# Performance work log

Measured on AMD Instinct MI355X. Metric: run time of the kernel, lower is better.

The kernel has to match this reference:

```python
import jax, jax.numpy as jnp
import numpy as np
from jax import lax

B, H, W = 512, 128, 128
ARCH = [1, 4096, 4096, 4096, 4096]
CONV_THRESH = 0.0
GRAPH_THRESH = 0.8
EMBED_DIM = 1


def setup_inputs() -> dict:
    key = jax.random.key(0)
    ks = jax.random.split(key, 16)
    inp = {
        "x": jax.random.normal(ks[0], (B, 1, H, W), dtype=jnp.float32),
        "conv_w": jax.random.normal(ks[1], (1, 1, 2, 2), dtype=jnp.float32) * 0.5,
        "conv_b": jax.random.normal(ks[2], (1,), dtype=jnp.float32) * 0.1,
        "rotation": jax.random.normal(ks[3], (EMBED_DIM, EMBED_DIM), dtype=jnp.float32),
        "entangle": jax.random.normal(ks[4], (EMBED_DIM, EMBED_DIM), dtype=jnp.float32),
    }
    # Linear params, torch convention W: [out_f, in_f]
    for i, (fi, fo) in enumerate(zip(ARCH[:-1], ARCH[1:])):
        inp[f"W{i+1}"] = jax.random.normal(ks[5 + 2 * i], (fo, fi), dtype=jnp.float32) / np.sqrt(fi)
        inp[f"b{i+1}"] = jax.random.normal(ks[6 + 2 * i], (fo,), dtype=jnp.float32) * 0.01
    return inp


def _forward(x, conv_w, conv_b, rotation, entangle, W1, b1, W2, b2, W3, b3, W4, b4):
    # ConvFilter: 2x2 valid conv, sigmoid(logits - thresh), mean over C,H,W -> [B]
    logits = lax.conv_general_dilated(
        x, conv_w, window_strides=(1, 1), padding="VALID",
        dimension_numbers=("NCHW", "OIHW", "NCHW"))
    logits = logits + conv_b.reshape(1, -1, 1, 1)
    conv_out = jax.nn.sigmoid(logits - CONV_THRESH).mean(axis=(1, 2, 3))  # [B]
    conv_vec = conv_out[:, None]  # [B, 1] -> embed_dim forced to 1

    # ClassicalSelfAttention (embed_dim = 1)
    q = conv_vec @ rotation                      # [B, 1]
    k = conv_vec @ entangle                      # [B, 1]
    scores = jax.nn.softmax((q @ k.T) / np.sqrt(EMBED_DIM).astype(np.float32), axis=-1)  # [B, B]
    attn_out = scores @ conv_vec                 # [B, 1]

    # tanh MLP stack
    out = attn_out
    acts = []
    for Wl, bl in ((W1, b1), (W2, b2), (W3, b3), (W4, b4)):
        out = jnp.tanh(out @ Wl.T + bl)          # [B, out_f]
        acts.append(out)

    # Vectorized fidelity adjacency over equal-shaped layer activations:
    # normalized Gram matrix squared, thresholded (replaces the O(L^2)
    # Python loop with .item() syncs in the source).
    S = jnp.stack([a.reshape(-1) for a in acts])                  # [L, B*4096]
    S_hat = S / (jnp.linalg.norm(S, axis=1, keepdims=True) + 1e-12)
    fid = (S_hat @ S_hat.T) ** 2                                   # [L, L]
    L = len(acts)
    weights = jnp.where(fid >= GRAPH_THRESH, 1.0, 0.0) * (1.0 - jnp.eye(L, dtype=fid.dtype))
    return out, weights


def reference(x, conv_w, conv_b, rotation, entangle, W1, b1, W2, b2, W3, b3, W4, b4):
    return _forward(x, conv_w, conv_b, rotation, entangle, W1, b1, W2, b2, W3, b3, W4, b4)
```

## Files before the change

### kernel.cpp

```cpp
#include <hip/hip_runtime.h>
#include <cmath>


#define NEL (512 * 4096)

typedef float  floatx4 __attribute__((ext_vector_type(4)));
typedef _Float16 halfx8 __attribute__((ext_vector_type(8)));
typedef _Float16 halfx4 __attribute__((ext_vector_type(4)));

__global__ __launch_bounds__(256) void conv_mean_kernel(
    const float* __restrict__ x, const float* __restrict__ cw,
    const float* __restrict__ cb, float* __restrict__ c_out)
{
  __shared__ float sbuf[4];
  const int b = blockIdx.x;
  const float w00 = cw[0], w01 = cw[1], w10 = cw[2], w11 = cw[3];
  const float bias = cb[0];
  const float* xb = x + (size_t)b * 128 * 128;
  float acc = 0.f;
  for (int idx = threadIdx.x; idx < 127 * 127; idx += 256) {
    int i = idx / 127;
    int j = idx - i * 127;
    const float* p = xb + i * 128 + j;
    float v = w00 * p[0] + w01 * p[1] + w10 * p[128] + w11 * p[129] + bias;
    acc += 1.0f / (1.0f + __expf(-v));
  }
  #pragma unroll
  for (int off = 32; off > 0; off >>= 1) acc += __shfl_down(acc, off, 64);
  const int lane = threadIdx.x & 63, wv = threadIdx.x >> 6;
  if (lane == 0) sbuf[wv] = acc;
  __syncthreads();
  if (threadIdx.x == 0)
    c_out[b] = (sbuf[0] + sbuf[1] + sbuf[2] + sbuf[3]) * (1.0f / 16129.0f);
}

__global__ __launch_bounds__(64) void attn_kernel(
    const float* __restrict__ c, const float* __restrict__ rot,
    const float* __restrict__ ent, float* __restrict__ attn)
{
  const int i = blockIdx.x;
  const int lane = threadIdx.x;
  const float t = rot[0] * ent[0] * c[i];
  float vals[8], cj[8];
  float mx = -1e30f;
  #pragma unroll
  for (int u = 0; u < 8; ++u) {
    float cv = c[lane + u * 64];
    cj[u] = cv;
    vals[u] = t * cv;
    mx = fmaxf(mx, vals[u]);
  }
  #pragma unroll
  for (int off = 32; off > 0; off >>= 1) mx = fmaxf(mx, __shfl_down(mx, off, 64));
  mx = __shfl(mx, 0, 64);
  float se = 0.f, sw = 0.f;
  #pragma unroll
  for (int u = 0; u < 8; ++u) {
    float e = __expf(vals[u] - mx);
    se += e;
    sw += e * cj[u];
  }
  #pragma unroll
  for (int off = 32; off > 0; off >>= 1) {
    se += __shfl_down(se, off, 64);
    sw += __shfl_down(sw, off, 64);
  }
  if (lane == 0) attn[i] = sw / se;
}

__global__ __launch_bounds__(256) void layer1_kernel(
    const float* __restrict__ attn, const float* __restrict__ W1,
    const float* __restrict__ b1, float* __restrict__ act1)
{
  const int o = blockIdx.x * 256 + threadIdx.x;
  const int i = blockIdx.y;
  act1[(size_t)i * 4096 + o] = tanhf(attn[i] * W1[o] + b1[o]);
}

#define BM 128
#define BN 128
#define BK 32
#define LDK 40

template<bool FUSE>
__global__ __launch_bounds__(256) void gemm_tanh_kernel(
    const float* __restrict__ A, const float* __restrict__ W,
    const float* __restrict__ bias, float* __restrict__ C)
{
  __shared__ _Float16 As[BM][LDK];
  __shared__ _Float16 Ws[BN][LDK];
  const int K = 4096, N = 4096;
  const int tid  = threadIdx.x;
  const int lane = tid & 63;
  const int wave = tid >> 6;
  const int wm = (wave >> 1) * 64;
  const int wn = (wave & 1) * 64;
  const int q  = lane >> 4;
  const int ml = lane & 15;
  const int tileM = blockIdx.y * BM;
  const int tileN = blockIdx.x * BN;
  const int Kslice = K / gridDim.z;
  const int kbeg = blockIdx.z * Kslice;
  float* Cb = FUSE ? C : C + (size_t)blockIdx.z * NEL;

  floatx4 acc[4][4] = {};

  for (int k0 = kbeg; k0 < kbeg + Kslice; k0 += BK) {
    __syncthreads();
    #pragma unroll
    for (int u = 0; u < 4; ++u) {
      const int id = tid + u * 256;
      const int r  = id >> 3;
      const int cc = (id & 7) << 2;
      const float4 av = *reinterpret_cast<const float4*>(
          A + (size_t)(tileM + r) * K + k0 + cc);
      halfx4 ha = { (_Float16)av.x, (_Float16)av.y, (_Float16)av.z, (_Float16)av.w };
      *reinterpret_cast<halfx4*>(&As[r][cc]) = ha;
      const float4 wvv = *reinterpret_cast<const float4*>(
          W + (size_t)(tileN + r) * K + k0 + cc);
      halfx4 hw = { (_Float16)wvv.x, (_Float16)wvv.y, (_Float16)wvv.z, (_Float16)wvv.w };
      *reinterpret_cast<halfx4*>(&Ws[r][cc]) = hw;
    }
    __syncthreads();

    halfx8 af[4], bf[4];
    #pragma unroll
    for (int i = 0; i < 4; ++i)
      af[i] = *reinterpret_cast<const halfx8*>(&As[wm + i * 16 + ml][q * 8]);
    #pragma unroll
    for (int j = 0; j < 4; ++j)
      bf[j] = *reinterpret_cast<const halfx8*>(&Ws[wn + j * 16 + ml][q * 8]);

    #pragma unroll
    for (int i = 0; i < 4; ++i)
      #pragma unroll
      for (int j = 0; j < 4; ++j)
        acc[i][j] = __builtin_amdgcn_mfma_f32_16x16x32_f16(af[i], bf[j], acc[i][j], 0, 0, 0);
  }

  #pragma unroll
  for (int i = 0; i < 4; ++i) {
    const int row0 = tileM + wm + i * 16 + q * 4;
    #pragma unroll
    for (int j = 0; j < 4; ++j) {
      const int col = tileN + wn + j * 16 + ml;
      if (FUSE) {
        const float bv = bias[col];
        #pragma unroll
        for (int r = 0; r < 4; ++r)
          Cb[(size_t)(row0 + r) * N + col] = tanhf(acc[i][j][r] + bv);
      } else {
        #pragma unroll
        for (int r = 0; r < 4; ++r)
          Cb[(size_t)(row0 + r) * N + col] = acc[i][j][r];
      }
    }
  }
}

__global__ __launch_bounds__(256) void combine_tanh_kernel(
    const float* __restrict__ part, const float* __restrict__ bias,
    float* __restrict__ outp)
{
  const int i4 = blockIdx.x * 256 + threadIdx.x;
  const floatx4* p4 = (const floatx4*)part;
  floatx4 s = p4[i4] + p4[NEL / 4 + i4] + p4[2 * (NEL / 4) + i4] + p4[3 * (NEL / 4) + i4];
  const floatx4 bv = ((const floatx4*)bias)[i4 & 1023];
  floatx4 o;
  #pragma unroll
  for (int r = 0; r < 4; ++r) o[r] = tanhf(s[r] + bv[r]);
  ((floatx4*)outp)[i4] = o;
}

__global__ __launch_bounds__(256) void fid_dots_kernel(
    const float* __restrict__ a1, const float* __restrict__ a2,
    const float* __restrict__ a3, const float* __restrict__ a4,
    float* __restrict__ D)
{
  __shared__ float sred[4][10];
  float s[10] = {0, 0, 0, 0, 0, 0, 0, 0, 0, 0};
  const int n4 = NEL / 4;
  const int stride = gridDim.x * blockDim.x;
  const floatx4* p1 = (const floatx4*)a1;
  const floatx4* p2 = (const floatx4*)a2;
  const floatx4* p3 = (const floatx4*)a3;
  const floatx4* p4 = (const floatx4*)a4;
  for (int i = blockIdx.x * 256 + threadIdx.x; i < n4; i += stride) {
    floatx4 v1 = p1[i], v2 = p2[i], v3 = p3[i], v4 = p4[i];
    #pragma unroll
    for (int r = 0; r < 4; ++r) {
      s[0] += v1[r] * v1[r]; s[1] += v1[r] * v2[r]; s[2] += v1[r] * v3[r];
      s[3] += v1[r] * v4[r]; s[4] += v2[r] * v2[r]; s[5] += v2[r] * v3[r];
      s[6] += v2[r] * v4[r]; s[7] += v3[r] * v3[r]; s[8] += v3[r] * v4[r];
      s[9] += v4[r] * v4[r];
    }
  }
  const int lane = threadIdx.x & 63, wv = threadIdx.x >> 6;
  #pragma unroll
  for (int p = 0; p < 10; ++p) {
    float v = s[p];
    #pragma unroll
    for (int off = 32; off > 0; off >>= 1) v += __shfl_down(v, off, 64);
    if (lane == 0) sred[wv][p] = v;
  }
  __syncthreads();
  if (threadIdx.x < 10) {
    float v = sred[0][threadIdx.x] + sred[1][threadIdx.x] +
              sred[2][threadIdx.x] + sred[3][threadIdx.x];
    atomicAdd(&D[threadIdx.x * 16], v);
  }
}

__global__ void finalize_kernel(const float* __restrict__ D, float* __restrict__ wout)
{
  const int i = threadIdx.x;
  if (i >= 16) return;
  const int p = i >> 2, qq = i & 3;
  const int a = p < qq ? p : qq;
  const int b = p < qq ? qq : p;
  const int base[4] = {0, 4, 7, 9};
  const float dpq = D[(base[a] + (b - a)) * 16];
  const float npv = sqrtf(D[base[p] * 16]) + 1e-12f;
  const float nqv = sqrtf(D[base[qq] * 16]) + 1e-12f;
  const float ch = dpq / (npv * nqv);
  const float fid = ch * ch;
  wout[i] = (fid >= 0.8f && p != qq) ? 1.0f : 0.0f;
}

extern "C" void kernel_launch(void* const* d_in, const int* in_sizes, int n_in,
                              void* d_out, int out_size, void* d_ws, size_t ws_size,
                              hipStream_t stream)
{
  const float* x   = (const float*)d_in[0];
  const float* cw  = (const float*)d_in[1];
  const float* cb  = (const float*)d_in[2];
  const float* rot = (const float*)d_in[3];
  const float* ent = (const float*)d_in[4];
  const float* W1  = (const float*)d_in[5];
  const float* b1  = (const float*)d_in[6];
  const float* W2  = (const float*)d_in[7];
  const float* b2  = (const float*)d_in[8];
  const float* W3  = (const float*)d_in[9];
  const float* b3  = (const float*)d_in[10];
  const float* W4  = (const float*)d_in[11];
  const float* b4  = (const float*)d_in[12];
  float* out = (float*)d_out;

  char*  ws    = (char*)d_ws;
  float* c_buf = (float*)(ws + 0);
  float* attn  = (float*)(ws + 2048);
  float* D     = (float*)(ws + 4096);
  float* act1  = (float*)(ws + 8192);
  float* act2  = act1 + NEL;
  float* act3  = act2 + NEL;
  float* part  = act3 + NEL;
  float* wout  = out + NEL;

  const size_t need = 8192 + (size_t)3 * NEL * 4 + (size_t)4 * NEL * 4;
  const bool splitk = ws_size >= need;

  hipMemsetAsync(D, 0, 10 * 16 * sizeof(float), stream);
  conv_mean_kernel<<<512, 256, 0, stream>>>(x, cw, cb, c_buf);
  attn_kernel<<<512, 64, 0, stream>>>(c_buf, rot, ent, attn);
  layer1_kernel<<<dim3(16, 512), 256, 0, stream>>>(attn, W1, b1, act1);

  if (splitk) {
    dim3 g(4096 / BN, 512 / BM, 4);
    const int cgrid = NEL / 4 / 256;
    gemm_tanh_kernel<false><<<g, 256, 0, stream>>>(act1, W2, nullptr, part);
    combine_tanh_kernel<<<cgrid, 256, 0, stream>>>(part, b2, act2);
    gemm_tanh_kernel<false><<<g, 256, 0, stream>>>(act2, W3, nullptr, part);
    combine_tanh_kernel<<<cgrid, 256, 0, stream>>>(part, b3, act3);
    gemm_tanh_kernel<false><<<g, 256, 0, stream>>>(act3, W4, nullptr, part);
    combine_tanh_kernel<<<cgrid, 256, 0, stream>>>(part, b4, out);
  } else {
    dim3 g(4096 / BN, 512 / BM, 1);
    gemm_tanh_kernel<true><<<g, 256, 0, stream>>>(act1, W2, b2, act2);
    gemm_tanh_kernel<true><<<g, 256, 0, stream>>>(act2, W3, b3, act3);
    gemm_tanh_kernel<true><<<g, 256, 0, stream>>>(act3, W4, b4, out);
  }

  fid_dots_kernel<<<256, 256, 0, stream>>>(act1, act2, act3, out, D);
  finalize_kernel<<<1, 64, 0, stream>>>(D, wout);
}
```

Baseline: 429.1 us.

## Register-prefetch GEMM tiles and add 8-way split-K path

```diff
diff --git a/kernel.cpp b/kernel.cpp
--- a/kernel.cpp
+++ b/kernel.cpp
@@ -6,7 +6,6 @@
 
 typedef float  floatx4 __attribute__((ext_vector_type(4)));
 typedef _Float16 halfx8 __attribute__((ext_vector_type(8)));
-typedef _Float16 halfx4 __attribute__((ext_vector_type(4)));
 
 __global__ __launch_bounds__(256) void conv_mean_kernel(
     const float* __restrict__ x, const float* __restrict__ cw,
@@ -101,27 +100,48 @@
   const int tileN = blockIdx.x * BN;
   const int Kslice = K / gridDim.z;
   const int kbeg = blockIdx.z * Kslice;
+  const int kend = kbeg + Kslice;
   float* Cb = FUSE ? C : C + (size_t)blockIdx.z * NEL;
 
   floatx4 acc[4][4] = {};
 
-  for (int k0 = kbeg; k0 < kbeg + Kslice; k0 += BK) {
+  const int r0  = tid >> 2;
+  const int cc0 = (tid & 3) << 3;
+
+  float4 pa[4], pw[4];
+  auto load_tile = [&](int k0) {
+    #pragma unroll
+    for (int u = 0; u < 2; ++u) {
+      const float* ap = A + (size_t)(tileM + r0 + u * 64) * K + k0 + cc0;
+      pa[2 * u]     = *reinterpret_cast<const float4*>(ap);
+      pa[2 * u + 1] = *reinterpret_cast<const float4*>(ap + 4);
+      const float* wp = W + (size_t)(tileN + r0 + u * 64) * K + k0 + cc0;
+      pw[2 * u]     = *reinterpret_cast<const float4*>(wp);
+      pw[2 * u + 1] = *reinterpret_cast<const float4*>(wp + 4);
+    }
+  };
+  auto store_tile = [&]() {
+    #pragma unroll
+    for (int u = 0; u < 2; ++u) {
+      halfx8 ha = { (_Float16)pa[2*u].x, (_Float16)pa[2*u].y,
+                    (_Float16)pa[2*u].z, (_Float16)pa[2*u].w,
+                    (_Float16)pa[2*u+1].x, (_Float16)pa[2*u+1].y,
+                    (_Float16)pa[2*u+1].z, (_Float16)pa[2*u+1].w };
+      *reinterpret_cast<halfx8*>(&As[r0 + u * 64][cc0]) = ha;
+      halfx8 hw = { (_Float16)pw[2*u].x, (_Float16)pw[2*u].y,
+                    (_Float16)pw[2*u].z, (_Float16)pw[2*u].w,
+                    (_Float16)pw[2*u+1].x, (_Float16)pw[2*u+1].y,
+                    (_Float16)pw[2*u+1].z, (_Float16)pw[2*u+1].w };
+      *reinterpret_cast<halfx8*>(&Ws[r0 + u * 64][cc0]) = hw;
+    }
+  };
+
+  load_tile(kbeg);
+  for (int k0 = kbeg; k0 < kend; k0 += BK) {
     __syncthreads();
-    #pragma unroll
-    for (int u = 0; u < 4; ++u) {
-      const int id = tid + u * 256;
-      const int r  = id >> 3;
-      const int cc = (id & 7) << 2;
-      const float4 av = *reinterpret_cast<const float4*>(
-          A + (size_t)(tileM + r) * K + k0 + cc);
-      halfx4 ha = { (_Float16)av.x, (_Float16)av.y, (_Float16)av.z, (_Float16)av.w };
-      *reinterpret_cast<halfx4*>(&As[r][cc]) = ha;
-      const float4 wvv = *reinterpret_cast<const float4*>(
-          W + (size_t)(tileN + r) * K + k0 + cc);
-      halfx4 hw = { (_Float16)wvv.x, (_Float16)wvv.y, (_Float16)wvv.z, (_Float16)wvv.w };
-      *reinterpret_cast<halfx4*>(&Ws[r][cc]) = hw;
-    }
+    store_tile();
     __syncthreads();
+    if (k0 + BK < kend) load_tile(k0 + BK);
 
     halfx8 af[4], bf[4];
     #pragma unroll
@@ -158,13 +178,16 @@
   }
 }
 
+template<int S>
 __global__ __launch_bounds__(256) void combine_tanh_kernel(
     const float* __restrict__ part, const float* __restrict__ bias,
     float* __restrict__ outp)
 {
   const int i4 = blockIdx.x * 256 + threadIdx.x;
   const floatx4* p4 = (const floatx4*)part;
-  floatx4 s = p4[i4] + p4[NEL / 4 + i4] + p4[2 * (NEL / 4) + i4] + p4[3 * (NEL / 4) + i4];
+  floatx4 s = p4[i4];
+  #pragma unroll
+  for (int z = 1; z < S; ++z) s += p4[(size_t)z * (NEL / 4) + i4];
   const floatx4 bv = ((const floatx4*)bias)[i4 & 1023];
   floatx4 o;
   #pragma unroll
@@ -256,23 +279,32 @@
   float* part  = act3 + NEL;
   float* wout  = out + NEL;
 
-  const size_t need = 8192 + (size_t)3 * NEL * 4 + (size_t)4 * NEL * 4;
-  const bool splitk = ws_size >= need;
+  const size_t base_need = 8192 + (size_t)3 * NEL * 4;
+  const bool sk8 = ws_size >= base_need + (size_t)8 * NEL * 4;
+  const bool sk4 = ws_size >= base_need + (size_t)4 * NEL * 4;
 
   hipMemsetAsync(D, 0, 10 * 16 * sizeof(float), stream);
   conv_mean_kernel<<<512, 256, 0, stream>>>(x, cw, cb, c_buf);
   attn_kernel<<<512, 64, 0, stream>>>(c_buf, rot, ent, attn);
   layer1_kernel<<<dim3(16, 512), 256, 0, stream>>>(attn, W1, b1, act1);
 
-  if (splitk) {
+  const int cgrid = NEL / 4 / 256;
+  if (sk8) {
+    dim3 g(4096 / BN, 512 / BM, 8);
+    gemm_tanh_kernel<false><<<g, 256, 0, stream>>>(act1, W2, nullptr, part);
+    combine_tanh_kernel<8><<<cgrid, 256, 0, stream>>>(part, b2, act2);
+    gemm_tanh_kernel<false><<<g, 256, 0, stream>>>(act2, W3, nullptr, part);
+    combine_tanh_kernel<8><<<cgrid, 256, 0, stream>>>(part, b3, act3);
+    gemm_tanh_kernel<false><<<g, 256, 0, stream>>>(act3, W4, nullptr, part);
+    combine_tanh_kernel<8><<<cgrid, 256, 0, stream>>>(part, b4, out);
+  } else if (sk4) {
     dim3 g(4096 / BN, 512 / BM, 4);
-    const int cgrid = NEL / 4 / 256;
     gemm_tanh_kernel<false><<<g, 256, 0, stream>>>(act1, W2, nullptr, part);
-    combine_tanh_kernel<<<cgrid, 256, 0, stream>>>(part, b2, act2);
+    combine_tanh_kernel<4><<<cgrid, 256, 0, stream>>>(part, b2, act2);
     gemm_tanh_kernel<false><<<g, 256, 0, stream>>>(act2, W3, nullptr, part);
-    combine_tanh_kernel<<<cgrid, 256, 0, stream>>>(part, b3, act3);
+    combine_tanh_kernel<4><<<cgrid, 256, 0, stream>>>(part, b3, act3);
     gemm_tanh_kernel<false><<<g, 256, 0, stream>>>(act3, W4, nullptr, part);
-    combine_tanh_kernel<<<cgrid, 256, 0, stream>>>(part, b4, out);
+    combine_tanh_kernel<4><<<cgrid, 256, 0, stream>>>(part, b4, out);
   } else {
     dim3 g(4096 / BN, 512 / BM, 1);
     gemm_tanh_kernel<true><<<g, 256, 0, stream>>>(act1, W2, b2, act2);
```

After: 456.2 us. 6.3% more time.
